# Optimization experiments

Measured on AMD Instinct MI355X. Metric: run time of the kernel, lower is better.

Reference implementation:

```python
import jax, jax.numpy as jnp
import numpy as np

B, T, D = 2, 2048, 2048
H = 16
HD = D // H  # 128
THETA = 10000.0


def setup_inputs() -> dict:
    key = jax.random.key(0)
    kx, kq, ko = jax.random.split(key, 3)
    x = jax.random.normal(kx, (B, T, D), dtype=jnp.float32)
    # store weights pre-transposed: y = x @ W
    Wqkv = jax.random.normal(kq, (D, 3 * D), dtype=jnp.float32) * (D ** -0.5)
    Wout = jax.random.normal(ko, (D, D), dtype=jnp.float32) * (D ** -0.5)
    # rotary cache: [T, HD//2, 2] = (cos, sin)
    inv_freq = 1.0 / (THETA ** (jnp.arange(0, HD, 2, dtype=jnp.float32) / HD))
    angles = jnp.arange(T, dtype=jnp.float32)[:, None] * inv_freq[None, :]
    freqs_cis = jnp.stack([jnp.cos(angles), jnp.sin(angles)], axis=-1)
    return {"x": x, "Wqkv": Wqkv, "Wout": Wout, "freqs_cis": freqs_cis}


def _apply_rotary(freqs_cis, t):
    # t: [B, H, T, HD]; freqs_cis: [T, HD//2, 2]
    b, h, s, d = t.shape
    tr = t.reshape(b, h, s, d // 2, 2)
    cos = freqs_cis[:s, :, 0]  # [T, HD//2]
    sin = freqs_cis[:s, :, 1]
    x0, x1 = tr[..., 0], tr[..., 1]
    o0 = x0 * cos - x1 * sin
    o1 = x1 * cos + x0 * sin
    return jnp.stack([o0, o1], axis=-1).reshape(b, h, s, d)


def reference(x, Wqkv, Wout, freqs_cis):
    b, s, d = x.shape
    qkv = x @ Wqkv  # [B, T, 3D]
    # 'B T (three h d) -> B three h T d'
    qkv = qkv.reshape(b, s, 3, H, HD).transpose(0, 2, 3, 1, 4)
    q, k, v = qkv[:, 0], qkv[:, 1], qkv[:, 2]  # each [B, H, T, HD]
    q = _apply_rotary(freqs_cis, q)
    k = _apply_rotary(freqs_cis, k)
    # causal SDPA
    scale = 1.0 / jnp.sqrt(jnp.asarray(HD, dtype=q.dtype))
    scores = jnp.einsum('bhqd,bhkd->bhqk', q, k) * scale
    causal = jnp.tril(jnp.ones((s, s), dtype=bool))
    scores = jnp.where(causal, scores, jnp.finfo(scores.dtype).min)
    probs = jax.nn.softmax(scores, axis=-1)
    out = jnp.einsum('bhqk,bhkd->bhqd', probs, v)  # [B, H, T, HD]
    out = out.transpose(0, 2, 1, 3).reshape(b, s, d)  # 'B h T d -> B T (h d)'
    return out @ Wout
```

## Files before the change

### kernel.cpp

```cpp
#include <hip/hip_runtime.h>
#include <math.h>

#define B_   2
#define T_   2048
#define D_   2048
#define H_   16
#define HD_  128
#define QKV_LD 6144
#define SCALE 0.08838834764831845f

typedef __attribute__((ext_vector_type(4))) float f32x4;
typedef __attribute__((ext_vector_type(8))) short bf16x8;

static __device__ __forceinline__ unsigned short f2bf(float f) {
    unsigned u = __builtin_bit_cast(unsigned, f);
    return (unsigned short)((u + 0x7FFFu + ((u >> 16) & 1u)) >> 16);
}
static __device__ __forceinline__ float bf2f(unsigned short h) {
    unsigned u = ((unsigned)h) << 16;
    return __builtin_bit_cast(float, u);
}

static __device__ __forceinline__ void gload_lds16(const void* g, void* l) {
    __builtin_amdgcn_global_load_lds(
        (const __attribute__((address_space(1))) unsigned int*)g,
        (__attribute__((address_space(3))) unsigned int*)l, 16, 0, 0);
}

__global__ __launch_bounds__(256)
void castx(const float* __restrict__ in, unsigned short* __restrict__ out) {
    size_t i = (size_t)blockIdx.x * 256 + threadIdx.x;
    const float4* p = (const float4*)in + 2 * i;
    float4 a = p[0], b = p[1];
    unsigned short tmp[8] = {f2bf(a.x), f2bf(a.y), f2bf(a.z), f2bf(a.w),
                             f2bf(b.x), f2bf(b.y), f2bf(b.z), f2bf(b.w)};
    ((uint4*)out)[i] = *(uint4*)tmp;
}

__global__ __launch_bounds__(256)
void wtrans(const float* __restrict__ W, unsigned short* __restrict__ Wt,
            int K, int N) {
    __shared__ float tile[64][65];
    int k0 = blockIdx.y * 64, n0 = blockIdx.x * 64;
    int t = threadIdx.x;
    #pragma unroll
    for (int i = 0; i < 4; ++i) {
        int f = t + 256 * i;
        int r = f >> 4, c4 = f & 15;
        float4 v = *(const float4*)(W + (size_t)(k0 + r) * N + n0 + c4 * 4);
        tile[r][c4 * 4 + 0] = v.x; tile[r][c4 * 4 + 1] = v.y;
        tile[r][c4 * 4 + 2] = v.z; tile[r][c4 * 4 + 3] = v.w;
    }
    __syncthreads();
    #pragma unroll
    for (int i = 0; i < 2; ++i) {
        int f = t + 256 * i;
        int r = f >> 3, c = f & 7;
        unsigned short tmp[8];
        #pragma unroll
        for (int j = 0; j < 8; ++j) tmp[j] = f2bf(tile[c * 8 + j][r]);
        *(uint4*)(Wt + (size_t)(n0 + r) * K + k0 + c * 8) = *(uint4*)tmp;
    }
}

template <bool OUT_BF16>
__global__ __launch_bounds__(256)
void gemm_bf16(const unsigned short* __restrict__ A,
               const unsigned short* __restrict__ Bt,
               float* __restrict__ Cf, unsigned short* __restrict__ Cb,
               int M, int N, int K) {
    __shared__ unsigned short As[128 * 64];
    __shared__ unsigned short Bs[128 * 64];
    int t = threadIdx.x;
    int wid = t >> 6, lane = t & 63;
    int wm = wid >> 1, wn = wid & 1;
    int lr = lane & 15, lg = lane >> 4;

    int nwg = gridDim.x * gridDim.y;
    int wg  = blockIdx.y * gridDim.x + blockIdx.x;
    int wgs = (wg & 7) * (nwg >> 3) + (wg >> 3);
    int m0 = (wgs / gridDim.x) * 128;
    int n0 = (wgs % gridDim.x) * 128;

    f32x4 acc[4][4];
    #pragma unroll
    for (int a = 0; a < 4; ++a)
        #pragma unroll
        for (int b = 0; b < 4; ++b)
            acc[a][b] = (f32x4){0.f, 0.f, 0.f, 0.f};

    for (int k0 = 0; k0 < K; k0 += 64) {
        #pragma unroll
        for (int i = 0; i < 4; ++i) {
            int c = (wid * 4 + i) * 64 + lane;
            int row = c >> 3, ch = (c & 7) ^ (row & 7);
            gload_lds16(A + (size_t)(m0 + row) * K + k0 + ch * 8,
                        (char*)As + (wid * 4 + i) * 1024);
            gload_lds16(Bt + (size_t)(n0 + row) * K + k0 + ch * 8,
                        (char*)Bs + (wid * 4 + i) * 1024);
        }
        __syncthreads();
        #pragma unroll
        for (int ks = 0; ks < 2; ++ks) {
            bf16x8 af[4], bfm[4];
            #pragma unroll
            for (int mb = 0; mb < 4; ++mb) {
                int row = wm * 64 + mb * 16 + lr;
                af[mb] = *(const bf16x8*)((const char*)As + row * 128 +
                          (((ks * 32 + lg * 8) * 2) ^ ((row & 7) << 4)));
            }
            #pragma unroll
            for (int nb = 0; nb < 4; ++nb) {
                int row = wn * 64 + nb * 16 + lr;
                bfm[nb] = *(const bf16x8*)((const char*)Bs + row * 128 +
                           (((ks * 32 + lg * 8) * 2) ^ ((row & 7) << 4)));
            }
            #pragma unroll
            for (int mb = 0; mb < 4; ++mb)
                #pragma unroll
                for (int nb = 0; nb < 4; ++nb)
                    acc[mb][nb] = __builtin_amdgcn_mfma_f32_16x16x32_bf16(
                        af[mb], bfm[nb], acc[mb][nb], 0, 0, 0);
        }
        __syncthreads();
    }
    #pragma unroll
    for (int mb = 0; mb < 4; ++mb)
        #pragma unroll
        for (int nb = 0; nb < 4; ++nb)
            #pragma unroll
            for (int r = 0; r < 4; ++r) {
                int row = m0 + wm * 64 + mb * 16 + lg * 4 + r;
                int col = n0 + wn * 64 + nb * 16 + lr;
                if (OUT_BF16)
                    Cb[(size_t)row * N + col] = f2bf(acc[mb][nb][r]);
                else
                    Cf[(size_t)row * N + col] = acc[mb][nb][r];
            }
}

__global__ __launch_bounds__(256)
void rope_qk(unsigned short* __restrict__ qkvb, const float* __restrict__ fc) {
    int gid = blockIdx.x * 256 + threadIdx.x;
    int ch  = gid & 15;
    int h   = (gid >> 4) & 15;
    int sel = (gid >> 8) & 1;
    int row = gid >> 9;
    int t   = row & (T_ - 1);

    unsigned short* p = qkvb + (size_t)row * QKV_LD + sel * D_ + h * HD_ + ch * 8;
    uint4 v = *(uint4*)p;
    unsigned short* s = (unsigned short*)&v;
    const float* f = fc + ((size_t)t * 64 + ch * 4) * 2;
    float4 fA = *(const float4*)f;
    float4 fB = *(const float4*)(f + 4);
    float x0 = bf2f(s[0]), x1 = bf2f(s[1]), x2 = bf2f(s[2]), x3 = bf2f(s[3]);
    float x4 = bf2f(s[4]), x5 = bf2f(s[5]), x6 = bf2f(s[6]), x7 = bf2f(s[7]);
    unsigned short o[8];
    o[0] = f2bf(x0 * fA.x - x1 * fA.y);
    o[1] = f2bf(x1 * fA.x + x0 * fA.y);
    o[2] = f2bf(x2 * fA.z - x3 * fA.w);
    o[3] = f2bf(x3 * fA.z + x2 * fA.w);
    o[4] = f2bf(x4 * fB.x - x5 * fB.y);
    o[5] = f2bf(x5 * fB.x + x4 * fB.y);
    o[6] = f2bf(x6 * fB.z - x7 * fB.w);
    o[7] = f2bf(x7 * fB.z + x6 * fB.w);
    *(uint4*)p = *(uint4*)o;
}

__global__ __launch_bounds__(256)
void vT_build(const unsigned short* __restrict__ qkvb,
              unsigned short* __restrict__ vT) {
    __shared__ unsigned short tile[128][72];
    int t0 = blockIdx.x * 64;
    int bh = blockIdx.y;
    int b = bh >> 4, h = bh & 15;
    int tid = threadIdx.x;
    #pragma unroll
    for (int i = 0; i < 4; ++i) {
        int f = tid + 256 * i;
        int tr = f >> 4, ch = f & 15;
        uint4 v = *(const uint4*)(qkvb +
            (size_t)(b * T_ + t0 + tr) * QKV_LD + 2 * D_ + h * HD_ + ch * 8);
        unsigned short* s = (unsigned short*)&v;
        #pragma unroll
        for (int j = 0; j < 8; ++j) tile[ch * 8 + j][tr] = s[j];
    }
    __syncthreads();
    #pragma unroll
    for (int i = 0; i < 4; ++i) {
        int f = tid + 256 * i;
        int d = f >> 3, ch = f & 7;
        uint4 v = *(uint4*)(&tile[d][ch * 8]);
        *(uint4*)(vT + ((size_t)(bh * 128 + d)) * T_ + t0 + ch * 8) = v;
    }
}

__global__ __launch_bounds__(256)
void attn_mfma(const unsigned short* __restrict__ qkvb,
               const unsigned short* __restrict__ vT,
               unsigned short* __restrict__ attnb) {
    __shared__ unsigned short Qs[64 * 128];
    __shared__ unsigned short Ks[2][64 * 128];
    __shared__ unsigned short Vts[2][128 * 64];

    int t = threadIdx.x;
    int wid = t >> 6, lane = t & 63;
    int lr = lane & 15, lg = lane >> 4;

    int wg  = blockIdx.x;
    int wgs = (wg & 7) * 128 + (wg >> 3);
    int bh  = wgs >> 5;
    int qt  = 31 - (wgs & 31);
    int b = bh >> 4, h = bh & 15;
    int qt0 = qt * 64;

    const unsigned short* qbase = qkvb + (size_t)(b * T_) * QKV_LD + h * HD_;
    const unsigned short* kbase = qbase + D_;
    const unsigned short* vbase = vT + (size_t)bh * 128 * T_;

    #pragma unroll
    for (int i = 0; i < 4; ++i) {
        int c = (wid * 4 + i) * 64 + lane;
        int row = c >> 4, ch = (c & 15) ^ (row & 7);
        gload_lds16(qbase + (size_t)(qt0 + row) * QKV_LD + ch * 8,
                    (char*)Qs + (wid * 4 + i) * 1024);
    }
    #pragma unroll
    for (int i = 0; i < 4; ++i) {
        int c = (wid * 4 + i) * 64 + lane;
        int rowk = c >> 4, chk = (c & 15) ^ (rowk & 7);
        gload_lds16(kbase + (size_t)rowk * QKV_LD + chk * 8,
                    (char*)Ks[0] + (wid * 4 + i) * 1024);
        int rowv = c >> 3, chv = (c & 7) ^ (rowv & 7);
        gload_lds16(vbase + (size_t)rowv * T_ + chv * 8,
                    (char*)Vts[0] + (wid * 4 + i) * 1024);
    }
    __syncthreads();

    bf16x8 qf[4];
    {
        int qrow = wid * 16 + lr;
        #pragma unroll
        for (int kd = 0; kd < 4; ++kd)
            qf[kd] = *(const bf16x8*)((const char*)Qs + qrow * 256 +
                       (((kd * 32 + lg * 8) * 2) ^ ((qrow & 7) << 4)));
    }
    __syncthreads();
    unsigned short* Ps = Qs;

    f32x4 o[8];
    #pragma unroll
    for (int nb = 0; nb < 8; ++nb) o[nb] = (f32x4){0.f, 0.f, 0.f, 0.f};
    float m_r = -1e30f, l_r = 0.f;
    const int qrow_g = qt0 + wid * 16 + lr;

    for (int kt = 0; kt <= qt; ++kt) {
        int cur = kt & 1;
        if (kt < qt) {
            #pragma unroll
            for (int i = 0; i < 4; ++i) {
                int c = (wid * 4 + i) * 64 + lane;
                int rowk = c >> 4, chk = (c & 15) ^ (rowk & 7);
                gload_lds16(kbase + (size_t)((kt + 1) * 64 + rowk) * QKV_LD + chk * 8,
                            (char*)Ks[cur ^ 1] + (wid * 4 + i) * 1024);
                int rowv = c >> 3, chv = (c & 7) ^ (rowv & 7);
                gload_lds16(vbase + (size_t)rowv * T_ + (kt + 1) * 64 + chv * 8,
                            (char*)Vts[cur ^ 1] + (wid * 4 + i) * 1024);
            }
        }
        const unsigned short* Kc = Ks[cur];
        const unsigned short* Vc = Vts[cur];

        f32x4 s[4];
        #pragma unroll
        for (int kb = 0; kb < 4; ++kb) s[kb] = (f32x4){0.f, 0.f, 0.f, 0.f};
        __builtin_amdgcn_s_setprio(1);
        #pragma unroll
        for (int kd = 0; kd < 4; ++kd) {
            #pragma unroll
            for (int kb = 0; kb < 4; ++kb) {
                int krow = kb * 16 + lr;
                bf16x8 kf = *(const bf16x8*)((const char*)Kc + krow * 256 +
                             (((kd * 32 + lg * 8) * 2) ^ ((krow & 7) << 4)));
                s[kb] = __builtin_amdgcn_mfma_f32_16x16x32_bf16(kf, qf[kd], s[kb], 0, 0, 0);
            }
        }
        __builtin_amdgcn_s_setprio(0);

        float sv[4][4];
        bool diag = (kt == qt);
        #pragma unroll
        for (int kb = 0; kb < 4; ++kb)
            #pragma unroll
            for (int r = 0; r < 4; ++r) {
                float v = s[kb][r] * SCALE;
                int key_g = kt * 64 + kb * 16 + 4 * lg + r;
                if (diag && key_g > qrow_g) v = -1e30f;
                sv[kb][r] = v;
            }
        float mt = -1e30f;
        #pragma unroll
        for (int kb = 0; kb < 4; ++kb)
            #pragma unroll
            for (int r = 0; r < 4; ++r) mt = fmaxf(mt, sv[kb][r]);
        mt = fmaxf(mt, __shfl_xor(mt, 16));
        mt = fmaxf(mt, __shfl_xor(mt, 32));

        bool defer = __all(mt - m_r <= 8.0f) != 0;
        float mnew  = defer ? m_r : fmaxf(m_r, mt);
        float alpha = defer ? 1.0f : __expf(m_r - mnew);

        float psum = 0.f;
        unsigned pw[4][2];
        #pragma unroll
        for (int kb = 0; kb < 4; ++kb) {
            float p0 = __expf(sv[kb][0] - mnew);
            float p1 = __expf(sv[kb][1] - mnew);
            float p2 = __expf(sv[kb][2] - mnew);
            float p3 = __expf(sv[kb][3] - mnew);
            psum += p0 + p1 + p2 + p3;
            pw[kb][0] = (unsigned)f2bf(p0) | ((unsigned)f2bf(p1) << 16);
            pw[kb][1] = (unsigned)f2bf(p2) | ((unsigned)f2bf(p3) << 16);
        }
        psum += __shfl_xor(psum, 16);
        psum += __shfl_xor(psum, 32);
        l_r = l_r * alpha + psum;
        m_r = mnew;

        if (!defer) {
            float a0 = __shfl(alpha, 4 * lg + 0, 16);
            float a1 = __shfl(alpha, 4 * lg + 1, 16);
            float a2 = __shfl(alpha, 4 * lg + 2, 16);
            float a3 = __shfl(alpha, 4 * lg + 3, 16);
            #pragma unroll
            for (int nb = 0; nb < 8; ++nb) {
                o[nb][0] *= a0; o[nb][1] *= a1; o[nb][2] *= a2; o[nb][3] *= a3;
            }
        }

        unsigned short* pbase = Ps + wid * 1152 + lr * 72;
        #pragma unroll
        for (int kb = 0; kb < 4; ++kb) {
            uint2 w; w.x = pw[kb][0]; w.y = pw[kb][1];
            *(uint2*)(pbase + kb * 16 + 4 * lg) = w;
        }
        __builtin_amdgcn_s_setprio(1);
        #pragma unroll
        for (int ks = 0; ks < 2; ++ks) {
            bf16x8 pa = *(const bf16x8*)(pbase + ks * 32 + 8 * lg);
            #pragma unroll
            for (int nb = 0; nb < 8; ++nb) {
                int vrow = nb * 16 + lr;
                bf16x8 vf = *(const bf16x8*)((const char*)Vc + vrow * 128 +
                             (((ks * 32 + lg * 8) * 2) ^ ((vrow & 7) << 4)));
                o[nb] = __builtin_amdgcn_mfma_f32_16x16x32_bf16(pa, vf, o[nb], 0, 0, 0);
            }
        }
        __builtin_amdgcn_s_setprio(0);
        __syncthreads();
    }

    float linv = 1.0f / l_r;
    float li0 = __shfl(linv, 4 * lg + 0, 16);
    float li1 = __shfl(linv, 4 * lg + 1, 16);
    float li2 = __shfl(linv, 4 * lg + 2, 16);
    float li3 = __shfl(linv, 4 * lg + 3, 16);
    #pragma unroll
    for (int nb = 0; nb < 8; ++nb) {
        float li[4] = {li0, li1, li2, li3};
        #pragma unroll
        for (int r = 0; r < 4; ++r) {
            int trow = qt0 + wid * 16 + 4 * lg + r;
            attnb[((size_t)(b * T_ + trow)) * D_ + h * HD_ + nb * 16 + lr] =
                f2bf(o[nb][r] * li[r]);
        }
    }
}

extern "C" void kernel_launch(void* const* d_in, const int* in_sizes, int n_in,
                              void* d_out, int out_size, void* d_ws, size_t ws_size,
                              hipStream_t stream) {
    const float* x    = (const float*)d_in[0];
    const float* Wqkv = (const float*)d_in[1];
    const float* Wout = (const float*)d_in[2];
    const float* fc   = (const float*)d_in[3];
    float* out = (float*)d_out;

    char* ws = (char*)d_ws;
    unsigned short* xb    = (unsigned short*)(ws);
    unsigned short* attnb = xb;
    unsigned short* WqkvT = (unsigned short*)(ws + 16777216);
    unsigned short* WoutT = (unsigned short*)(ws + 41943040);
    unsigned short* qkvb  = (unsigned short*)(ws + 50331648);
    unsigned short* vT    = (unsigned short*)(ws + 100663296);

    dim3 blk(256);

    castx<<<4096, blk, 0, stream>>>(x, xb);
    wtrans<<<dim3(96, 32), blk, 0, stream>>>(Wqkv, WqkvT, 2048, 6144);
    wtrans<<<dim3(32, 32), blk, 0, stream>>>(Wout, WoutT, 2048, 2048);

    gemm_bf16<true><<<dim3(48, 32), blk, 0, stream>>>(xb, WqkvT, nullptr, qkvb,
                                                      4096, 6144, 2048);
    rope_qk<<<8192, blk, 0, stream>>>(qkvb, fc);
    vT_build<<<dim3(32, 32), blk, 0, stream>>>(qkvb, vT);
    attn_mfma<<<1024, blk, 0, stream>>>(qkvb, vT, attnb);
    gemm_bf16<false><<<dim3(16, 32), blk, 0, stream>>>(attnb, WoutT, out, nullptr,
                                                       4096, 2048, 2048);
}
```

Baseline: 424.2 us.

## Replace GEMM with triple-buffered 256x128 tile pipelined kernel using 8 waves

Replaces the single-buffered 128x128 bf16 GEMM with a 512-thread, 256x128-tile kernel that keeps three LDS buffers and prefetches the tile two k-steps ahead using global_load_lds. Each k-step is split into two halves that interleave LDS fragment reads, async stage issue and MFMA bursts, separated by barriers and with raised wave priority around the MFMA blocks. The aim is to hide global memory latency and raise MFMA utilization in both the QKV and output projections. In exchange it uses more LDS (about 144 KB per block) and depends on hand-placed vmcnt waits being correct.

```diff
diff --git a/kernel.cpp b/kernel.cpp
--- a/kernel.cpp
+++ b/kernel.cpp
@@ -64,74 +64,136 @@
 }
 
 template <bool OUT_BF16>
-__global__ __launch_bounds__(256)
-void gemm_bf16(const unsigned short* __restrict__ A,
-               const unsigned short* __restrict__ Bt,
-               float* __restrict__ Cf, unsigned short* __restrict__ Cb,
-               int M, int N, int K) {
-    __shared__ unsigned short As[128 * 64];
-    __shared__ unsigned short Bs[128 * 64];
-    int t = threadIdx.x;
-    int wid = t >> 6, lane = t & 63;
-    int wm = wid >> 1, wn = wid & 1;
-    int lr = lane & 15, lg = lane >> 4;
-
-    int nwg = gridDim.x * gridDim.y;
-    int wg  = blockIdx.y * gridDim.x + blockIdx.x;
-    int wgs = (wg & 7) * (nwg >> 3) + (wg >> 3);
-    int m0 = (wgs / gridDim.x) * 128;
-    int n0 = (wgs % gridDim.x) * 128;
-
-    f32x4 acc[4][4];
-    #pragma unroll
-    for (int a = 0; a < 4; ++a)
-        #pragma unroll
-        for (int b = 0; b < 4; ++b)
-            acc[a][b] = (f32x4){0.f, 0.f, 0.f, 0.f};
-
-    for (int k0 = 0; k0 < K; k0 += 64) {
-        #pragma unroll
-        for (int i = 0; i < 4; ++i) {
-            int c = (wid * 4 + i) * 64 + lane;
-            int row = c >> 3, ch = (c & 7) ^ (row & 7);
-            gload_lds16(A + (size_t)(m0 + row) * K + k0 + ch * 8,
-                        (char*)As + (wid * 4 + i) * 1024);
-            gload_lds16(Bt + (size_t)(n0 + row) * K + k0 + ch * 8,
-                        (char*)Bs + (wid * 4 + i) * 1024);
-        }
-        __syncthreads();
-        #pragma unroll
-        for (int ks = 0; ks < 2; ++ks) {
-            bf16x8 af[4], bfm[4];
-            #pragma unroll
-            for (int mb = 0; mb < 4; ++mb) {
-                int row = wm * 64 + mb * 16 + lr;
-                af[mb] = *(const bf16x8*)((const char*)As + row * 128 +
-                          (((ks * 32 + lg * 8) * 2) ^ ((row & 7) << 4)));
-            }
-            #pragma unroll
-            for (int nb = 0; nb < 4; ++nb) {
-                int row = wn * 64 + nb * 16 + lr;
-                bfm[nb] = *(const bf16x8*)((const char*)Bs + row * 128 +
-                           (((ks * 32 + lg * 8) * 2) ^ ((row & 7) << 4)));
-            }
-            #pragma unroll
-            for (int mb = 0; mb < 4; ++mb)
+__global__ __launch_bounds__(512, 2)
+void gemm_p2(const unsigned short* __restrict__ A,
+             const unsigned short* __restrict__ Bt,
+             float* __restrict__ Cf, unsigned short* __restrict__ Cb,
+             int M, int N, int K) {
+    __shared__ unsigned short As[3][256 * 64];
+    __shared__ unsigned short Bs[3][128 * 64];
+
+    const int t = threadIdx.x;
+    const int wid = t >> 6, lane = t & 63;
+    const int wm = wid >> 2, wn = wid & 3;
+    const int lr = lane & 15, lg = lane >> 4;
+
+    const int gx  = N >> 7;
+    const int nwg = gridDim.x;
+    const int wg  = blockIdx.x;
+    const int wgs = (wg & 7) * (nwg >> 3) + (wg >> 3);
+    const int m0  = (wgs / gx) * 256;
+    const int n0  = (wgs % gx) * 128;
+
+    const int nt = K >> 6;
+
+    const int sr  = lane >> 3;
+    const int sc  = lane & 7;
+    auto stageA = [&](int kt, int buf) {
+        const unsigned short* src = A + (size_t)m0 * K + kt * 64;
+        #pragma unroll
+        for (int j = 0; j < 4; ++j) {
+            int r = (wid * 4 + j) * 8 + sr;
+            int ch = sc ^ (r & 7);
+            gload_lds16(src + (size_t)r * K + ch * 8,
+                        (char*)As[buf] + (wid * 4 + j) * 1024);
+        }
+    };
+    auto stageB = [&](int kt, int buf) {
+        const unsigned short* src = Bt + (size_t)n0 * K + kt * 64;
+        #pragma unroll
+        for (int j = 0; j < 2; ++j) {
+            int r = (wid * 2 + j) * 8 + sr;
+            int ch = sc ^ (r & 7);
+            gload_lds16(src + (size_t)r * K + ch * 8,
+                        (char*)Bs[buf] + (wid * 2 + j) * 1024);
+        }
+    };
+    auto ldA = [&](int buf, int mb, int ks) -> bf16x8 {
+        int row = wm * 128 + mb * 16 + lr;
+        return *(const bf16x8*)((const char*)As[buf] + row * 128 +
+                (((ks * 32 + lg * 8) * 2) ^ ((row & 7) << 4)));
+    };
+    auto ldB = [&](int buf, int nb, int ks) -> bf16x8 {
+        int row = wn * 32 + nb * 16 + lr;
+        return *(const bf16x8*)((const char*)Bs[buf] + row * 128 +
+                (((ks * 32 + lg * 8) * 2) ^ ((row & 7) << 4)));
+    };
+
+    f32x4 acc[8][2];
+    #pragma unroll
+    for (int mb = 0; mb < 8; ++mb)
+        #pragma unroll
+        for (int nb = 0; nb < 2; ++nb)
+            acc[mb][nb] = (f32x4){0.f, 0.f, 0.f, 0.f};
+
+    stageA(0, 0); stageB(0, 0);
+    stageA(1, 1); stageB(1, 1);
+    asm volatile("s_waitcnt vmcnt(6)" ::: "memory");
+    __builtin_amdgcn_s_barrier();
+
+    for (int kt = 0; kt < nt; ++kt) {
+        const int buf  = kt % 3;
+        const int nbuf = (kt + 2) % 3;
+        const bool pf  = (kt + 2) < nt;
+
+        bf16x8 a0[4][2], bb[2][2];
+        #pragma unroll
+        for (int mb = 0; mb < 4; ++mb)
+            #pragma unroll
+            for (int ks = 0; ks < 2; ++ks) a0[mb][ks] = ldA(buf, mb, ks);
+        #pragma unroll
+        for (int nb = 0; nb < 2; ++nb)
+            #pragma unroll
+            for (int ks = 0; ks < 2; ++ks) bb[nb][ks] = ldB(buf, nb, ks);
+        if (pf) stageA(kt + 2, nbuf);
+        __builtin_amdgcn_s_barrier();
+        __builtin_amdgcn_sched_barrier(0);
+        __builtin_amdgcn_s_setprio(1);
+        #pragma unroll
+        for (int mb = 0; mb < 4; ++mb)
+            #pragma unroll
+            for (int nb = 0; nb < 2; ++nb)
                 #pragma unroll
-                for (int nb = 0; nb < 4; ++nb)
+                for (int ks = 0; ks < 2; ++ks)
                     acc[mb][nb] = __builtin_amdgcn_mfma_f32_16x16x32_bf16(
-                        af[mb], bfm[nb], acc[mb][nb], 0, 0, 0);
-        }
-        __syncthreads();
-    }
-    #pragma unroll
-    for (int mb = 0; mb < 4; ++mb)
-        #pragma unroll
-        for (int nb = 0; nb < 4; ++nb)
+                        a0[mb][ks], bb[nb][ks], acc[mb][nb], 0, 0, 0);
+        __builtin_amdgcn_s_setprio(0);
+        __builtin_amdgcn_s_barrier();
+
+        bf16x8 a1[4][2];
+        #pragma unroll
+        for (int mb = 0; mb < 4; ++mb)
+            #pragma unroll
+            for (int ks = 0; ks < 2; ++ks) a1[mb][ks] = ldA(buf, mb + 4, ks);
+        if (pf) stageB(kt + 2, nbuf);
+        __builtin_amdgcn_s_barrier();
+        __builtin_amdgcn_sched_barrier(0);
+        __builtin_amdgcn_s_setprio(1);
+        #pragma unroll
+        for (int mb = 0; mb < 4; ++mb)
+            #pragma unroll
+            for (int nb = 0; nb < 2; ++nb)
+                #pragma unroll
+                for (int ks = 0; ks < 2; ++ks)
+                    acc[mb + 4][nb] = __builtin_amdgcn_mfma_f32_16x16x32_bf16(
+                        a1[mb][ks], bb[nb][ks], acc[mb + 4][nb], 0, 0, 0);
+        __builtin_amdgcn_s_setprio(0);
+        if (kt + 2 < nt) {
+            asm volatile("s_waitcnt vmcnt(6)" ::: "memory");
+        } else if (kt + 1 < nt) {
+            asm volatile("s_waitcnt vmcnt(0)" ::: "memory");
+        }
+        __builtin_amdgcn_s_barrier();
+    }
+
+    #pragma unroll
+    for (int mb = 0; mb < 8; ++mb)
+        #pragma unroll
+        for (int nb = 0; nb < 2; ++nb)
             #pragma unroll
             for (int r = 0; r < 4; ++r) {
-                int row = m0 + wm * 64 + mb * 16 + lg * 4 + r;
-                int col = n0 + wn * 64 + nb * 16 + lr;
+                int row = m0 + wm * 128 + mb * 16 + lg * 4 + r;
+                int col = n0 + wn * 32 + nb * 16 + lr;
                 if (OUT_BF16)
                     Cb[(size_t)row * N + col] = f2bf(acc[mb][nb][r]);
                 else
@@ -401,11 +463,11 @@
     wtrans<<<dim3(96, 32), blk, 0, stream>>>(Wqkv, WqkvT, 2048, 6144);
     wtrans<<<dim3(32, 32), blk, 0, stream>>>(Wout, WoutT, 2048, 2048);
 
-    gemm_bf16<true><<<dim3(48, 32), blk, 0, stream>>>(xb, WqkvT, nullptr, qkvb,
-                                                      4096, 6144, 2048);
+    gemm_p2<true><<<768, 512, 0, stream>>>(xb, WqkvT, nullptr, qkvb,
+                                           4096, 6144, 2048);
     rope_qk<<<8192, blk, 0, stream>>>(qkvb, fc);
     vT_build<<<dim3(32, 32), blk, 0, stream>>>(qkvb, vT);
     attn_mfma<<<1024, blk, 0, stream>>>(qkvb, vT, attnb);
-    gemm_bf16<false><<<dim3(16, 32), blk, 0, stream>>>(attnb, WoutT, out, nullptr,
-                                                       4096, 2048, 2048);
-}
+    gemm_p2<false><<<256, 512, 0, stream>>>(attnb, WoutT, out, nullptr,
+                                            4096, 2048, 2048);
+}
```

Result: no change. 423.5 us (-0.2%).

## Add 256x256 eight-wave ping-pong GEMM for the QKV projection

Applied to the files above, without the earlier changes.

Introduces a new bf16 MFMA GEMM with 256x256 tiles, 512 threads and a double-buffered LDS pipeline. Global-to-LDS loads for the next k-tile are interleaved with four MFMA phases, coordinated by barriers, explicit waitcnt and setprio. The QKV projection now uses this kernel in place of the 128x128 one. The aim is more data reuse per tile and better overlap of memory with compute. In exchange it uses 128KB of LDS, has fewer workgroups (384), and writes the output with uncoalesced scalar bf16 stores.

```diff
diff --git a/kernel.cpp b/kernel.cpp
--- a/kernel.cpp
+++ b/kernel.cpp
@@ -61,6 +61,158 @@
         for (int j = 0; j < 8; ++j) tmp[j] = f2bf(tile[c * 8 + j][r]);
         *(uint4*)(Wt + (size_t)(n0 + r) * K + k0 + c * 8) = *(uint4*)tmp;
     }
+}
+
+#define PHASE_MFMA(MG, NG, BF)                                                 \
+    __builtin_amdgcn_s_barrier();                                              \
+    asm volatile("s_waitcnt lgkmcnt(0)" ::: "memory");                         \
+    __builtin_amdgcn_sched_barrier(0);                                         \
+    __builtin_amdgcn_s_setprio(1);                                             \
+    _Pragma("unroll")                                                          \
+    for (int mb4 = 0; mb4 < 4; ++mb4)                                          \
+        _Pragma("unroll")                                                      \
+        for (int nb2 = 0; nb2 < 2; ++nb2)                                      \
+            _Pragma("unroll")                                                  \
+            for (int ks = 0; ks < 2; ++ks)                                     \
+                acc[(MG)*4 + mb4][(NG)*2 + nb2] =                              \
+                    __builtin_amdgcn_mfma_f32_16x16x32_bf16(                   \
+                        af[mb4*2 + ks], BF[nb2*2 + ks],                        \
+                        acc[(MG)*4 + mb4][(NG)*2 + nb2], 0, 0, 0);             \
+    __builtin_amdgcn_s_setprio(0);
+
+template <bool OUT_BF16>
+__global__ __launch_bounds__(512, 2)
+void gemm_8p(const unsigned short* __restrict__ A,
+             const unsigned short* __restrict__ Bt,
+             float* __restrict__ Cf, unsigned short* __restrict__ Cb,
+             int M, int N, int K) {
+    __shared__ unsigned short LDS[8 * 8192];
+
+    const int t = threadIdx.x;
+    const int wid = t >> 6, lane = t & 63;
+    const int wm = wid >> 2, wn = wid & 3;
+    const int lr = lane & 15, lg = lane >> 4;
+
+    const int gx  = N >> 8;
+    const int nwg = gridDim.x;
+    const int wg  = blockIdx.x;
+    const int wgs = (wg & 7) * (nwg >> 3) + (wg >> 3);
+    const int m0  = (wgs / gx) << 8;
+    const int n0  = (wgs % gx) << 8;
+
+    const unsigned short* Ab = A + (size_t)m0 * K;
+    const unsigned short* Bb = Bt + (size_t)n0 * K;
+    const int sr = lane >> 3, sc = lane & 7;
+
+    auto stage = [&](int s, int ab, int h, int kt) {
+        const unsigned short* base = ab ? Bb : Ab;
+        char* dst = (char*)LDS + (((s * 2 + ab) * 2 + h) << 14);
+        #pragma unroll
+        for (int j = 0; j < 2; ++j) {
+            int blk = wid * 2 + j;
+            int r   = blk * 8 + sr;
+            int ch  = sc ^ (r & 7);
+            gload_lds16(base + (size_t)(h * 128 + r) * K + kt * 64 + ch * 8,
+                        dst + blk * 1024);
+        }
+    };
+    auto ldsA = [&](int s, int mb, int ks) -> bf16x8 {
+        const char* rg = (const char*)LDS + (((s * 2 + 0) * 2 + wm) << 14);
+        int lrow = mb * 16 + lr;
+        return *(const bf16x8*)(rg + lrow * 128 +
+                (((ks * 32 + lg * 8) * 2) ^ ((lrow & 7) << 4)));
+    };
+    auto ldsB = [&](int s, int nb, int ks) -> bf16x8 {
+        const char* rg = (const char*)LDS + (((s * 2 + 1) * 2 + (wn >> 1)) << 14);
+        int lrow = (wn & 1) * 64 + nb * 16 + lr;
+        return *(const bf16x8*)(rg + lrow * 128 +
+                (((ks * 32 + lg * 8) * 2) ^ ((lrow & 7) << 4)));
+    };
+
+    f32x4 acc[8][4];
+    #pragma unroll
+    for (int i = 0; i < 8; ++i)
+        #pragma unroll
+        for (int jn = 0; jn < 4; ++jn)
+            acc[i][jn] = (f32x4){0.f, 0.f, 0.f, 0.f};
+
+    bf16x8 af[8], b0f[4], b1f[4];
+    auto loadAsub = [&](int s, int mg) {
+        #pragma unroll
+        for (int i = 0; i < 4; ++i) {
+            af[i*2 + 0] = ldsA(s, mg*4 + i, 0);
+            af[i*2 + 1] = ldsA(s, mg*4 + i, 1);
+        }
+    };
+    auto loadBsub = [&](int s, int ng, bf16x8* bf) {
+        #pragma unroll
+        for (int i = 0; i < 2; ++i) {
+            bf[i*2 + 0] = ldsB(s, ng*2 + i, 0);
+            bf[i*2 + 1] = ldsB(s, ng*2 + i, 1);
+        }
+    };
+
+    const int nt    = K >> 6;
+    const int nIter = nt >> 1;
+
+    stage(0,0,0,0); stage(0,0,1,0); stage(0,1,0,0); stage(0,1,1,0);
+    stage(1,1,0,1); stage(1,1,1,1);
+    asm volatile("s_waitcnt vmcnt(4)" ::: "memory");
+    __builtin_amdgcn_s_barrier();
+
+    for (int j = 0; j < nIter; ++j) {
+        const int a = 2*j, b = 2*j + 1;
+        const bool more = (j + 1 < nIter);
+
+        loadAsub(0, 0); loadBsub(0, 0, b0f);
+        stage(1, 0, 0, b);
+        PHASE_MFMA(0, 0, b0f)
+        __builtin_amdgcn_s_barrier();
+        loadBsub(0, 1, b1f);
+        stage(1, 0, 1, b);
+        PHASE_MFMA(0, 1, b1f)
+        __builtin_amdgcn_s_barrier();
+        loadAsub(0, 1);
+        if (more) stage(0, 1, 0, a + 2);
+        PHASE_MFMA(1, 0, b0f)
+        __builtin_amdgcn_s_barrier();
+        if (more) stage(0, 1, 1, a + 2);
+        PHASE_MFMA(1, 1, b1f)
+        if (more) { asm volatile("s_waitcnt vmcnt(4)" ::: "memory"); }
+        else      { asm volatile("s_waitcnt vmcnt(0)" ::: "memory"); }
+        __builtin_amdgcn_s_barrier();
+
+        loadAsub(1, 0); loadBsub(1, 0, b0f);
+        if (more) stage(0, 0, 0, a + 2);
+        PHASE_MFMA(0, 0, b0f)
+        __builtin_amdgcn_s_barrier();
+        loadBsub(1, 1, b1f);
+        if (more) stage(0, 0, 1, a + 2);
+        PHASE_MFMA(0, 1, b1f)
+        __builtin_amdgcn_s_barrier();
+        loadAsub(1, 1);
+        if (more) stage(1, 1, 0, b + 2);
+        PHASE_MFMA(1, 0, b0f)
+        __builtin_amdgcn_s_barrier();
+        if (more) stage(1, 1, 1, b + 2);
+        PHASE_MFMA(1, 1, b1f)
+        if (more) { asm volatile("s_waitcnt vmcnt(4)" ::: "memory"); }
+        __builtin_amdgcn_s_barrier();
+    }
+
+    #pragma unroll
+    for (int mb = 0; mb < 8; ++mb)
+        #pragma unroll
+        for (int nb = 0; nb < 4; ++nb)
+            #pragma unroll
+            for (int r = 0; r < 4; ++r) {
+                int row = m0 + wm * 128 + mb * 16 + lg * 4 + r;
+                int col = n0 + wn * 64 + nb * 16 + lr;
+                if (OUT_BF16)
+                    Cb[(size_t)row * N + col] = f2bf(acc[mb][nb][r]);
+                else
+                    Cf[(size_t)row * N + col] = acc[mb][nb][r];
+            }
 }
 
 template <bool OUT_BF16>
@@ -401,8 +553,8 @@
     wtrans<<<dim3(96, 32), blk, 0, stream>>>(Wqkv, WqkvT, 2048, 6144);
     wtrans<<<dim3(32, 32), blk, 0, stream>>>(Wout, WoutT, 2048, 2048);
 
-    gemm_bf16<true><<<dim3(48, 32), blk, 0, stream>>>(xb, WqkvT, nullptr, qkvb,
-                                                      4096, 6144, 2048);
+    gemm_8p<true><<<384, 512, 0, stream>>>(xb, WqkvT, nullptr, qkvb,
+                                           4096, 6144, 2048);
     rope_qk<<<8192, blk, 0, stream>>>(qkvb, fc);
     vT_build<<<dim3(32, 32), blk, 0, stream>>>(qkvb, vT);
     attn_mfma<<<1024, blk, 0, stream>>>(qkvb, vT, attnb);
```

New measurement: 416.0 us. About the same (-1.9%).
